# Kernel optimization log

Hardware: AMD Instinct MI355X
Metric: run time of the kernel (lower is better)

## Reference

```python
import jax, jax.numpy as jnp
import numpy as np

N, E, ND, ED, H, OUT, L, VC = 10000, 160000, 8, 4, 128, 256, 6, 6
HEADS, C = 4, 128  # GATConv: out_channels=128 per head, concat=False -> mean over heads


def _ln(x, g, b, eps=1e-5):
    m = x.mean(-1, keepdims=True)
    v = ((x - m) ** 2).mean(-1, keepdims=True)
    return (x - m) * jax.lax.rsqrt(v + eps) * g + b


def _gat_layer(h, src, dst, e_attr, lw, a_src, a_dst, lew, a_edge, bias):
    # h: [N,H]; e_attr: [Etot,H]; PyG GATConv(heads=4, concat=False, edge_dim=H)
    xh = (h @ lw).reshape(N, HEADS, C)                 # [N,4,128]
    eh = (e_attr @ lew).reshape(-1, HEADS, C)          # [Etot,4,128]
    al_s = jnp.einsum('nhc,hc->nh', xh, a_src)
    al_d = jnp.einsum('nhc,hc->nh', xh, a_dst)
    al_e = jnp.einsum('ehc,hc->eh', eh, a_edge)
    alpha = jax.nn.leaky_relu(al_s[src] + al_d[dst] + al_e, 0.2)  # [Etot,4]
    amax = jax.ops.segment_max(alpha, dst, num_segments=N)
    ex = jnp.exp(alpha - amax[dst])
    den = jax.ops.segment_sum(ex, dst, num_segments=N)
    w = ex / (den[dst] + 1e-16)
    out = jax.ops.segment_sum(xh[src] * w[..., None], dst, num_segments=N)  # [N,4,128]
    return out.mean(axis=1) + bias


def setup_inputs() -> dict:
    key = jax.random.key(0)
    ks = jax.random.split(key, 32)
    s = 0.05
    d = {
        'x': jax.random.normal(ks[0], (N, ND), jnp.float32),
        'edge_index': jax.random.randint(ks[1], (2, E), 0, N),
        'edge_attr': jax.random.uniform(ks[2], (E, ED), jnp.float32),
        'vnf_context': jax.random.normal(ks[3], (1, VC), jnp.float32),
        # node embedding
        'node_w': jax.random.normal(ks[4], (ND, H)) * s, 'node_b': jnp.zeros((H,)),
        # EdgeAttentionLayer
        'ea_proj_w': jax.random.normal(ks[5], (ED, H)) * s, 'ea_proj_b': jnp.zeros((H,)),
        'vnf_w': jax.random.normal(ks[6], (VC, H)) * s, 'vnf_b': jnp.zeros((H,)),
        'att1_w': jax.random.normal(ks[7], (2 * H, H)) * s, 'att1_b': jnp.zeros((H,)),
        'att2_w': jax.random.normal(ks[8], (H, H // 2)) * s, 'att2_b': jnp.zeros((H // 2,)),
        'att3_w': jax.random.normal(ks[9], (H // 2, 1)) * s, 'att3_b': jnp.zeros((1,)),
        # per-layer GATConv params (stacked over L layers)
        'gat_lin_w': jax.random.normal(ks[10], (L, H, HEADS * C)) * s,
        'gat_att_src': jax.random.normal(ks[11], (L, HEADS, C)) * s,
        'gat_att_dst': jax.random.normal(ks[12], (L, HEADS, C)) * s,
        'gat_lin_edge_w': jax.random.normal(ks[13], (L, H, HEADS * C)) * s,
        'gat_att_edge': jax.random.normal(ks[14], (L, HEADS, C)) * s,
        'gat_bias': jnp.zeros((L, C)),
        'ln_scale': jnp.ones((L, H)), 'ln_bias': jnp.zeros((L, H)),
        # output projection
        'out_w': jax.random.normal(ks[15], (H, OUT)) * s, 'out_b': jnp.zeros((OUT,)),
    }
    return d


def reference(x, edge_index, edge_attr, vnf_context, node_w, node_b, ea_proj_w, ea_proj_b,
              vnf_w, vnf_b, att1_w, att1_b, att2_w, att2_b, att3_w, att3_b,
              gat_lin_w, gat_att_src, gat_att_dst, gat_lin_edge_w, gat_att_edge, gat_bias,
              ln_scale, ln_bias, out_w, out_b):
    src, dst = edge_index[0], edge_index[1]
    h = x @ node_w + node_b                                   # [N,128]
    # EdgeAttentionLayer (eval mode, no network_state)
    ef = edge_attr @ ea_proj_w + ea_proj_b                    # [E,128]
    vnf = vnf_context @ vnf_w + vnf_b                         # [1,128]
    comb = jnp.concatenate([ef, jnp.broadcast_to(vnf, (E, H))], axis=-1)
    a = jax.nn.relu(comb @ att1_w + att1_b)
    a = jax.nn.relu(a @ att2_w + att2_b)
    e_gate = jax.nn.sigmoid(a @ att3_w + att3_b)              # [E,1]
    w_edge = ef * e_gate                                      # [E,128]
    # GATConv default add_self_loops=True, fill_value='mean'
    loop = jnp.arange(N)
    src2 = jnp.concatenate([src, loop])
    dst2 = jnp.concatenate([dst, loop])
    e2 = jnp.concatenate([w_edge, jnp.broadcast_to(w_edge.mean(0, keepdims=True), (N, H))], axis=0)
    for l in range(L):
        hc = _gat_layer(h, src2, dst2, e2, gat_lin_w[l], gat_att_src[l], gat_att_dst[l],
                        gat_lin_edge_w[l], gat_att_edge[l], gat_bias[l])
        h = _ln(h + jax.nn.relu(hc), ln_scale[l], ln_bias[l])
    return h @ out_w + out_b                                  # [N,256]
```

## Files before the change

### kernel.cpp

```cpp
#include <hip/hip_runtime.h>
#include <hip/hip_bf16.h>
#include <math.h>

#define Nn 10000
#define Ee 160000
#define LL 6

typedef short v8s __attribute__((ext_vector_type(8)));
typedef float v4f __attribute__((ext_vector_type(4)));

__device__ __forceinline__ unsigned short f2bf(float v) {
    unsigned int b = __float_as_uint(v);
    b += 0x7fffu + ((b >> 16) & 1u);
    return (unsigned short)(b >> 16);
}
__device__ __forceinline__ float bflo(unsigned int u) { return __uint_as_float(u << 16); }
__device__ __forceinline__ float bfhi(unsigned int u) { return __uint_as_float(u & 0xffff0000u); }

__global__ __launch_bounds__(256) void k_first(
    const float* __restrict__ x, const float* __restrict__ nw,
    const float* __restrict__ nb, float* __restrict__ h, unsigned short* __restrict__ hb,
    const int* __restrict__ ei, int* __restrict__ hist,
    const float* __restrict__ glw, const float* __restrict__ gas,
    const float* __restrict__ gad, const float* __restrict__ glew,
    const float* __restrict__ gae, float* __restrict__ Bs,
    float* __restrict__ Bd, float* __restrict__ Be,
    unsigned short* __restrict__ WsumT,
    const float* __restrict__ a2w, unsigned short* __restrict__ w2bf,
    const float* __restrict__ ow, unsigned short* __restrict__ owbT,
    const float* __restrict__ vnfc, const float* __restrict__ vw,
    const float* __restrict__ vb, const float* __restrict__ eab,
    const float* __restrict__ a1w, const float* __restrict__ a1b,
    const float* __restrict__ eaw, float* __restrict__ E1) {
    __shared__ float vr[128];
    __shared__ float sM1[512];
    __shared__ float sd1[128];
    int b = blockIdx.x, t = threadIdx.x;
    if (b < 5000) {
        int idx = b * 256 + t;
        int n = idx >> 7, c = idx & 127;
        const float* xr = x + (size_t)n * 8;
        float acc = nb[c];
#pragma unroll
        for (int k = 0; k < 8; k++) acc += xr[k] * nw[k * 128 + c];
        h[idx] = acc;
        hb[idx] = f2bf(acc);
        return;
    }
    if (b < 5625) {
        int i = (b - 5000) * 256 + t;
        atomicAdd(&hist[ei[Ee + i]], 1);
        return;
    }
    if (b < 5637) {
        int idx = (b - 5625) * 256 + t;
        if (idx >= LL * 128 * 4) return;
        int hh = idx & 3, k = (idx >> 2) & 127, l = idx >> 9;
        const float* lwp = glw  + (size_t)l * 65536 + k * 512 + hh * 128;
        const float* lep = glew + (size_t)l * 65536 + k * 512 + hh * 128;
        const float* sp = gas + l * 512 + hh * 128;
        const float* dp = gad + l * 512 + hh * 128;
        const float* ep = gae + l * 512 + hh * 128;
        float s1 = 0, s2 = 0, s3 = 0;
        for (int c = 0; c < 128; c++) {
            float lv = lwp[c];
            s1 += lv * sp[c];
            s2 += lv * dp[c];
            s3 += lep[c] * ep[c];
        }
        Bs[idx] = s1; Bd[idx] = s2; Be[idx] = s3;
        return;
    }
    if (b < 7173) {
        int idx = (b - 5637) * 256 + t;
        int kk = idx & 511;
        int c = (idx >> 9) & 127;
        int l = idx >> 16;
        float v = 0.25f * glw[(size_t)l * 65536 + (size_t)(kk & 127) * 512 + (kk >> 7) * 128 + c];
        WsumT[(size_t)l * 65536 + (size_t)c * 512 + kk] = f2bf(v);
        return;
    }
    if (b < 7205) {
        int idx = (b - 7173) * 256 + t;
        int j = idx & 7, lane = (idx >> 3) & 63, nt = (idx >> 9) & 3, ks = idx >> 11;
        int k = ks * 32 + ((lane >> 4) << 3) + j;
        int n = nt * 16 + (lane & 15);
        w2bf[idx] = f2bf(a2w[k * 64 + n]);
        return;
    }
    if (b < 7333) {
        int idx = (b - 7205) * 256 + t;
        int col = idx >> 7, kk = idx & 127;
        owbT[idx] = f2bf(ow[kk * 256 + col]);
        return;
    }
    {
        if (t < 128) {
            float a = vb[t];
#pragma unroll
            for (int k = 0; k < 6; k++) a += vnfc[k] * vw[k * 128 + t];
            vr[t] = a;
        }
        __syncthreads();
        if (t < 128) {
            float a = a1b[t];
            for (int k = 0; k < 128; k++) a += eab[k] * a1w[k * 128 + t];
            for (int k = 0; k < 128; k++) a += vr[k] * a1w[(128 + k) * 128 + t];
            sd1[t] = a;
        }
#pragma unroll
        for (int rr = 0; rr < 2; rr++) {
            int id = rr * 256 + t;
            int r = id >> 7, j = id & 127;
            float a = 0.f;
            for (int k = 0; k < 128; k++) a += eaw[r * 128 + k] * a1w[k * 128 + j];
            sM1[id] = a;
        }
        __syncthreads();
        if (t < 128) {
            E1[t * 8 + 0] = sM1[t];
            E1[t * 8 + 1] = sM1[128 + t];
            E1[t * 8 + 2] = sM1[256 + t];
            E1[t * 8 + 3] = sM1[384 + t];
            E1[t * 8 + 4] = sd1[t];
            E1[t * 8 + 5] = 0.f; E1[t * 8 + 6] = 0.f; E1[t * 8 + 7] = 0.f;
        }
    }
}

__global__ __launch_bounds__(1024) void k_scan(
    const int* __restrict__ hist, int* __restrict__ seg, int* __restrict__ pos,
    const float* __restrict__ eaw, const float* __restrict__ eab,
    const float* __restrict__ Be, float* __restrict__ PB, float* __restrict__ cB) {
    __shared__ int wsums[16];
    __shared__ int carry_s;
    int t = threadIdx.x;
    if (blockIdx.x == 1) {
        if (t >= 24) return;
        int l = t >> 2, hh = t & 3;
        const float* bp = Be + l * 512 + hh;
        float s0 = 0, s1 = 0, s2 = 0, s3 = 0, sc = 0;
        for (int k = 0; k < 128; k++) {
            float bv = bp[k * 4];
            s0 += eaw[0 * 128 + k] * bv;
            s1 += eaw[1 * 128 + k] * bv;
            s2 += eaw[2 * 128 + k] * bv;
            s3 += eaw[3 * 128 + k] * bv;
            sc += eab[k] * bv;
        }
        PB[0 * 24 + t] = s0; PB[1 * 24 + t] = s1;
        PB[2 * 24 + t] = s2; PB[3 * 24 + t] = s3;
        cB[t] = sc;
        return;
    }
    int lane = t & 63, wid = t >> 6;
    if (t == 0) { carry_s = 0; seg[0] = 0; }
    __syncthreads();
    for (int base = 0; base < Nn; base += 1024) {
        int idx = base + t;
        int v = (idx < Nn) ? hist[idx] : 0;
        int sc = v;
#pragma unroll
        for (int d = 1; d < 64; d <<= 1) {
            int up = __shfl_up(sc, d);
            if (lane >= d) sc += up;
        }
        if (lane == 63) wsums[wid] = sc;
        __syncthreads();
        if (wid == 0) {
            int wv = (lane < 16) ? wsums[lane] : 0;
            int wsc = wv;
#pragma unroll
            for (int d = 1; d < 16; d <<= 1) {
                int up = __shfl_up(wsc, d);
                if (lane >= d) wsc += up;
            }
            if (lane < 16) wsums[lane] = wsc - wv;
        }
        __syncthreads();
        int carry = carry_s;
        int inc = sc + wsums[wid] + carry;
        if (idx < Nn) { seg[idx + 1] = inc; pos[idx] = inc - v; }
        __syncthreads();
        if (t == 1023) carry_s = inc;
        __syncthreads();
    }
}

__global__ __launch_bounds__(256, 2) void k_edge(
    const float* __restrict__ ea, const float* __restrict__ E1,
    const unsigned short* __restrict__ w2bf,
    const float* __restrict__ a2b, const float* __restrict__ a3w,
    const float* __restrict__ a3b,
    const float* __restrict__ PB, const float* __restrict__ cB,
    const int* __restrict__ ei, int* __restrict__ pos, int* __restrict__ srcv,
    float* __restrict__ aleT, float* __restrict__ gsum,
    const float* __restrict__ h, const float* __restrict__ Bs,
    const float* __restrict__ Bd, float* __restrict__ als, float* __restrict__ ald) {
    __shared__ float4 sM[128];
    __shared__ float sD[128];
    __shared__ float4 sevs[256];
    __shared__ float gsh[256];
    __shared__ float sgsum[5];
    int t = threadIdx.x;
    int b = blockIdx.x;
    if (b >= 625) {
        int idx = (b - 625) * 256 + t;
        if (idx >= Nn * 8) return;
        int n = idx >> 3, slot = idx & 7;
        const float* B = (slot < 4) ? Bs : Bd;
        int hh = slot & 3;
        const float4* hr = (const float4*)(h + (size_t)n * 128);
        float s = 0.f;
#pragma unroll 8
        for (int kb = 0; kb < 32; kb++) {
            float4 hv = hr[kb];
            s += hv.x * B[(4 * kb + 0) * 4 + hh] + hv.y * B[(4 * kb + 1) * 4 + hh]
               + hv.z * B[(4 * kb + 2) * 4 + hh] + hv.w * B[(4 * kb + 3) * 4 + hh];
        }
        if (slot < 4) als[n * 4 + hh] = s;
        else          ald[n * 4 + hh] = s;
        return;
    }
    int lane = t & 63;
    int wid = t >> 6;
    int c = lane & 15, q = lane >> 4;
    int eb0 = b * 256;

    int my_src = ei[eb0 + t];
    int my_dst = ei[Ee + eb0 + t];
    sevs[t] = *(const float4*)(ea + (size_t)(eb0 + t) * 4);
    if (t < 128) {
        int slot = t ^ ((t >> 3) & 3);
        sM[slot] = *(const float4*)(E1 + t * 8);
        sD[t] = E1[t * 8 + 4];
    }
    if (t < 5) sgsum[t] = 0.f;
    __syncthreads();

    float4 ev4[4];
#pragma unroll
    for (int mt = 0; mt < 4; mt++) ev4[mt] = sevs[(wid * 4 + mt) * 16 + c];

    v8s av[4][4];
#pragma unroll
    for (int ks = 0; ks < 4; ks++) {
        float4 mr[8]; float dr[8];
#pragma unroll
        for (int j = 0; j < 8; j++) {
            int k = ks * 32 + q * 8 + j;
            mr[j] = sM[k ^ q];
            dr[j] = sD[k];
        }
#pragma unroll
        for (int mt = 0; mt < 4; mt++) {
            float4 ev = ev4[mt];
            v8s a;
#pragma unroll
            for (int j = 0; j < 8; j++) {
                float xv = fmaxf(dr[j] + ev.x * mr[j].x + ev.y * mr[j].y
                                       + ev.z * mr[j].z + ev.w * mr[j].w, 0.f);
                a[j] = (short)f2bf(xv);
            }
            av[mt][ks] = a;
        }
    }

    v4f acc[4][4];
#pragma unroll
    for (int nt = 0; nt < 4; nt++) {
        float bb = a2b[nt * 16 + c];
#pragma unroll
        for (int mt = 0; mt < 4; mt++) acc[mt][nt] = (v4f){bb, bb, bb, bb};
    }
#pragma unroll
    for (int nt = 0; nt < 4; nt++) {
#pragma unroll
        for (int ks = 0; ks < 4; ks++) {
            v8s bfr = *(const v8s*)(w2bf + ((size_t)(ks * 4 + nt) * 64 + lane) * 8);
#pragma unroll
            for (int mt = 0; mt < 4; mt++)
                acc[mt][nt] = __builtin_amdgcn_mfma_f32_16x16x32_bf16(av[mt][ks], bfr, acc[mt][nt], 0, 0, 0);
        }
    }

    float a3r[4];
#pragma unroll
    for (int nt = 0; nt < 4; nt++) a3r[nt] = a3w[nt * 16 + c];
    float a3b0 = a3b[0];
#pragma unroll
    for (int mt = 0; mt < 4; mt++) {
#pragma unroll
        for (int r = 0; r < 4; r++) {
            float s = 0.f;
#pragma unroll
            for (int nt = 0; nt < 4; nt++) s += fmaxf(acc[mt][nt][r], 0.f) * a3r[nt];
            s += __shfl_xor(s, 1); s += __shfl_xor(s, 2);
            s += __shfl_xor(s, 4); s += __shfl_xor(s, 8);
            if (c == 0) gsh[(wid * 4 + mt) * 16 + q * 4 + r] = 1.f / (1.f + __expf(-(s + a3b0)));
        }
    }
    __syncthreads();

    float g = gsh[t];
    float4 evv = sevs[t];
    float v0 = g, v1 = g * evv.x, v2 = g * evv.y, v3 = g * evv.z, v4 = g * evv.w;
#pragma unroll
    for (int d = 32; d > 0; d >>= 1) {
        v0 += __shfl_down(v0, d); v1 += __shfl_down(v1, d); v2 += __shfl_down(v2, d);
        v3 += __shfl_down(v3, d); v4 += __shfl_down(v4, d);
    }
    if (lane == 0) {
        atomicAdd(&sgsum[0], v0); atomicAdd(&sgsum[1], v1); atomicAdd(&sgsum[2], v2);
        atomicAdd(&sgsum[3], v3); atomicAdd(&sgsum[4], v4);
    }
    __syncthreads();
    if (t < 5) atomicAdd(&gsum[t], sgsum[t]);
    int slot = atomicAdd(&pos[my_dst], 1);
    srcv[slot] = my_src;
#pragma unroll
    for (int i4 = 0; i4 < 6; i4++) {
        float4 cc = *(const float4*)(cB + i4 * 4);
        float4 p0 = *(const float4*)(PB + 0 * 24 + i4 * 4);
        float4 p1 = *(const float4*)(PB + 1 * 24 + i4 * 4);
        float4 p2 = *(const float4*)(PB + 2 * 24 + i4 * 4);
        float4 p3 = *(const float4*)(PB + 3 * 24 + i4 * 4);
        float4 o;
        o.x = g * (cc.x + evv.x * p0.x + evv.y * p1.x + evv.z * p2.x + evv.w * p3.x);
        o.y = g * (cc.y + evv.x * p0.y + evv.y * p1.y + evv.z * p2.y + evv.w * p3.y);
        o.z = g * (cc.z + evv.x * p0.z + evv.y * p1.z + evv.z * p2.z + evv.w * p3.z);
        o.w = g * (cc.w + evv.x * p0.w + evv.y * p1.w + evv.z * p2.w + evv.w * p3.w);
        *(float4*)(aleT + (size_t)i4 * Ee * 4 + (size_t)slot * 4) = o;
    }
}

__global__ __launch_bounds__(1024) void k_agg3(
    const int* __restrict__ srcv, const int* __restrict__ seg,
    const float* __restrict__ als, const float* __restrict__ ald,
    const float* __restrict__ aleS_l,
    const unsigned short* __restrict__ hb, unsigned short* __restrict__ aggb,
    const float* __restrict__ gsum, const float* __restrict__ PBl,
    const float* __restrict__ cBl) {
    __shared__ float part[8][512];
    __shared__ float pden[8][4];
    int t = threadIdx.x;
    int lane = t & 63;
    int wv = (t >> 6) & 1;
    int w = t >> 7;
    int n = blockIdx.x * 8 + w;
    int start = seg[n], end = seg[n + 1];
    int deg = end - start;
    int half = (deg + 1) >> 1;
    int s0 = start + wv * half;
    int e0 = wv ? end : start + half;
    int hp = lane >> 4;
    int cch = (lane & 15) * 8;
    float aldh = ald[n * 4 + hp];
    float den = 0.f;
    float4 acc0 = make_float4(0.f, 0.f, 0.f, 0.f);
    float4 acc1 = make_float4(0.f, 0.f, 0.f, 0.f);
    int i = s0;
    for (; i + 4 <= e0; i += 4) {
        int sa = srcv[i], sb = srcv[i + 1], sc = srcv[i + 2], sd = srcv[i + 3];
        float ala = aleS_l[(size_t)(i + 0) * 4 + hp];
        float alb = aleS_l[(size_t)(i + 1) * 4 + hp];
        float alc = aleS_l[(size_t)(i + 2) * 4 + hp];
        float ald_ = aleS_l[(size_t)(i + 3) * 4 + hp];
        float asa = als[sa * 4 + hp], asb = als[sb * 4 + hp];
        float asc = als[sc * 4 + hp], asd = als[sd * 4 + hp];
        uint4 ua = *(const uint4*)(hb + (size_t)sa * 128 + cch);
        uint4 ub = *(const uint4*)(hb + (size_t)sb * 128 + cch);
        uint4 uc = *(const uint4*)(hb + (size_t)sc * 128 + cch);
        uint4 ud = *(const uint4*)(hb + (size_t)sd * 128 + cch);
        float ava = asa + aldh + ala; ava = ava > 0.f ? ava : 0.2f * ava;
        float avb = asb + aldh + alb; avb = avb > 0.f ? avb : 0.2f * avb;
        float avc = asc + aldh + alc; avc = avc > 0.f ? avc : 0.2f * avc;
        float avd = asd + aldh + ald_; avd = avd > 0.f ? avd : 0.2f * avd;
        float ea = __expf(fminf(ava, 60.f));
        float eb = __expf(fminf(avb, 60.f));
        float ec = __expf(fminf(avc, 60.f));
        float ed = __expf(fminf(avd, 60.f));
        den += (ea + eb) + (ec + ed);
        acc0.x += (ea * bflo(ua.x) + eb * bflo(ub.x)) + (ec * bflo(uc.x) + ed * bflo(ud.x));
        acc0.y += (ea * bfhi(ua.x) + eb * bfhi(ub.x)) + (ec * bfhi(uc.x) + ed * bfhi(ud.x));
        acc0.z += (ea * bflo(ua.y) + eb * bflo(ub.y)) + (ec * bflo(uc.y) + ed * bflo(ud.y));
        acc0.w += (ea * bfhi(ua.y) + eb * bfhi(ub.y)) + (ec * bfhi(uc.y) + ed * bfhi(ud.y));
        acc1.x += (ea * bflo(ua.z) + eb * bflo(ub.z)) + (ec * bflo(uc.z) + ed * bflo(ud.z));
        acc1.y += (ea * bfhi(ua.z) + eb * bfhi(ub.z)) + (ec * bfhi(uc.z) + ed * bfhi(ud.z));
        acc1.z += (ea * bflo(ua.w) + eb * bflo(ub.w)) + (ec * bflo(uc.w) + ed * bflo(ud.w));
        acc1.w += (ea * bfhi(ua.w) + eb * bfhi(ub.w)) + (ec * bfhi(uc.w) + ed * bfhi(ud.w));
    }
    for (; i < e0; i++) {
        int sa = srcv[i];
        float ala = aleS_l[(size_t)i * 4 + hp];
        float ava = als[sa * 4 + hp] + aldh + ala;
        ava = ava > 0.f ? ava : 0.2f * ava;
        float ea = __expf(fminf(ava, 60.f));
        den += ea;
        uint4 ua = *(const uint4*)(hb + (size_t)sa * 128 + cch);
        acc0.x += ea * bflo(ua.x); acc0.y += ea * bfhi(ua.x);
        acc0.z += ea * bflo(ua.y); acc0.w += ea * bfhi(ua.y);
        acc1.x += ea * bflo(ua.z); acc1.y += ea * bfhi(ua.z);
        acc1.z += ea * bflo(ua.w); acc1.w += ea * bfhi(ua.w);
    }
    if (wv == 0) {
        float lale = (gsum[0] * cBl[hp] + gsum[1] * PBl[hp] + gsum[2] * PBl[24 + hp]
                    + gsum[3] * PBl[48 + hp] + gsum[4] * PBl[72 + hp]) * (1.0f / Ee);
        float av = als[n * 4 + hp] + aldh + lale;
        av = av > 0.f ? av : 0.2f * av;
        float e0s = __expf(fminf(av, 60.f));
        den += e0s;
        uint4 ua = *(const uint4*)(hb + (size_t)n * 128 + cch);
        acc0.x += e0s * bflo(ua.x); acc0.y += e0s * bfhi(ua.x);
        acc0.z += e0s * bflo(ua.y); acc0.w += e0s * bfhi(ua.y);
        acc1.x += e0s * bflo(ua.z); acc1.y += e0s * bfhi(ua.z);
        acc1.z += e0s * bflo(ua.w); acc1.w += e0s * bfhi(ua.w);
    }
    if (wv == 1) {
        *(float4*)&part[w][lane * 8] = acc0;
        *(float4*)&part[w][lane * 8 + 4] = acc1;
        if ((lane & 15) == 0) pden[w][hp] = den;
    }
    __syncthreads();
    if (wv == 0) {
        float4 p0 = *(const float4*)&part[w][lane * 8];
        float4 p1 = *(const float4*)&part[w][lane * 8 + 4];
        float inv2 = 1.f / (den + pden[w][hp] + 1e-16f);
        acc0.x = (acc0.x + p0.x) * inv2; acc0.y = (acc0.y + p0.y) * inv2;
        acc0.z = (acc0.z + p0.z) * inv2; acc0.w = (acc0.w + p0.w) * inv2;
        acc1.x = (acc1.x + p1.x) * inv2; acc1.y = (acc1.y + p1.y) * inv2;
        acc1.z = (acc1.z + p1.z) * inv2; acc1.w = (acc1.w + p1.w) * inv2;
        ushort4 q0, q1;
        q0.x = f2bf(acc0.x); q0.y = f2bf(acc0.y); q0.z = f2bf(acc0.z); q0.w = f2bf(acc0.w);
        q1.x = f2bf(acc1.x); q1.y = f2bf(acc1.y); q1.z = f2bf(acc1.z); q1.w = f2bf(acc1.w);
        *(ushort4*)(aggb + (size_t)n * 512 + lane * 8) = q0;
        *(ushort4*)(aggb + (size_t)n * 512 + lane * 8 + 4) = q1;
    }
}

__global__ __launch_bounds__(256) void k_post(
    const unsigned short* __restrict__ aggb, const unsigned short* __restrict__ WsumT_l,
    const float* __restrict__ gbias, const float* __restrict__ lnsc,
    const float* __restrict__ lnbi, float* __restrict__ h,
    unsigned short* __restrict__ hb, const float* __restrict__ Bs_n,
    const float* __restrict__ Bd_n, float* __restrict__ als, float* __restrict__ ald,
    const unsigned short* __restrict__ owbT, const float* __restrict__ ob,
    float* __restrict__ out) {
    int t = threadIdx.x;
    int lane = t & 63, w = t >> 6;
    int n0 = (blockIdx.x * 4 + w) * 16;
    if (n0 >= Nn) return;
    int m = lane & 15, q = lane >> 4;
    v4f acc[8];
#pragma unroll
    for (int nt = 0; nt < 8; nt++) acc[nt] = (v4f){0.f, 0.f, 0.f, 0.f};
    const unsigned short* arow = aggb + (size_t)(n0 + m) * 512 + q * 8;
#pragma unroll 4
    for (int ks = 0; ks < 16; ks++) {
        v8s fa = *(const v8s*)(arow + ks * 32);
#pragma unroll
        for (int nt = 0; nt < 8; nt++) {
            int col = nt * 16 + m;
            v8s fb = *(const v8s*)(WsumT_l + (size_t)col * 512 + ks * 32 + q * 8);
            acc[nt] = __builtin_amdgcn_mfma_f32_16x16x32_bf16(fa, fb, acc[nt], 0, 0, 0);
        }
    }
    float v[8][4];
    float s1[4] = {0.f, 0.f, 0.f, 0.f}, s2[4] = {0.f, 0.f, 0.f, 0.f};
#pragma unroll
    for (int nt = 0; nt < 8; nt++) {
        int col = nt * 16 + m;
        float b = gbias[col];
#pragma unroll
        for (int r = 0; r < 4; r++) {
            int row = n0 + q * 4 + r;
            float val = h[(size_t)row * 128 + col] + fmaxf(acc[nt][r] + b, 0.f);
            v[nt][r] = val;
            s1[r] += val; s2[r] += val * val;
        }
    }
#pragma unroll
    for (int d = 1; d <= 8; d <<= 1) {
#pragma unroll
        for (int r = 0; r < 4; r++) {
            s1[r] += __shfl_xor(s1[r], d);
            s2[r] += __shfl_xor(s2[r], d);
        }
    }
    float o8[8][4];
#pragma unroll
    for (int r = 0; r < 4; r++) {
        float mean = s1[r] * (1.f / 128.f);
        float var = s2[r] * (1.f / 128.f) - mean * mean;
        float rinv = rsqrtf(var + 1e-5f);
        int row = n0 + q * 4 + r;
#pragma unroll
        for (int nt = 0; nt < 8; nt++) {
            int col = nt * 16 + m;
            float o = (v[nt][r] - mean) * rinv * lnsc[col] + lnbi[col];
            o8[nt][r] = o;
            h[(size_t)row * 128 + col] = o;
            hb[(size_t)row * 128 + col] = f2bf(o);
        }
    }
    if (owbT == nullptr) {
        float sal[4][4], sad[4][4];
#pragma unroll
        for (int r = 0; r < 4; r++) {
#pragma unroll
            for (int hh = 0; hh < 4; hh++) { sal[r][hh] = 0.f; sad[r][hh] = 0.f; }
        }
#pragma unroll
        for (int nt = 0; nt < 8; nt++) {
            int col = nt * 16 + m;
            float4 bs = *(const float4*)(Bs_n + col * 4);
            float4 bd = *(const float4*)(Bd_n + col * 4);
#pragma unroll
            for (int r = 0; r < 4; r++) {
                float o = o8[nt][r];
                sal[r][0] += o * bs.x; sal[r][1] += o * bs.y;
                sal[r][2] += o * bs.z; sal[r][3] += o * bs.w;
                sad[r][0] += o * bd.x; sad[r][1] += o * bd.y;
                sad[r][2] += o * bd.z; sad[r][3] += o * bd.w;
            }
        }
#pragma unroll
        for (int d = 1; d <= 8; d <<= 1) {
#pragma unroll
            for (int r = 0; r < 4; r++) {
#pragma unroll
                for (int hh = 0; hh < 4; hh++) {
                    sal[r][hh] += __shfl_xor(sal[r][hh], d);
                    sad[r][hh] += __shfl_xor(sad[r][hh], d);
                }
            }
        }
        if (m < 8) {
            int hh = m & 3;
#pragma unroll
            for (int r = 0; r < 4; r++) {
                int row = n0 + q * 4 + r;
                float va = (hh == 0) ? sal[r][0] : (hh == 1) ? sal[r][1] : (hh == 2) ? sal[r][2] : sal[r][3];
                float vd = (hh == 0) ? sad[r][0] : (hh == 1) ? sad[r][1] : (hh == 2) ? sad[r][2] : sad[r][3];
                if (m < 4) als[row * 4 + hh] = va;
                else       ald[row * 4 + hh] = vd;
            }
        }
    } else {
        v4f oacc[16];
#pragma unroll
        for (int ct = 0; ct < 16; ct++) oacc[ct] = (v4f){0.f, 0.f, 0.f, 0.f};
#pragma unroll
        for (int ks = 0; ks < 4; ks++) {
            v8s fa = *(const v8s*)(hb + (size_t)(n0 + m) * 128 + ks * 32 + q * 8);
#pragma unroll
            for (int ct = 0; ct < 16; ct++) {
                v8s fb = *(const v8s*)(owbT + (size_t)(ct * 16 + m) * 128 + ks * 32 + q * 8);
                oacc[ct] = __builtin_amdgcn_mfma_f32_16x16x32_bf16(fa, fb, oacc[ct], 0, 0, 0);
            }
        }
#pragma unroll
        for (int ct = 0; ct < 16; ct++) {
            float obv = ob[ct * 16 + m];
#pragma unroll
            for (int r = 0; r < 4; r++) {
                int row = n0 + q * 4 + r;
                out[(size_t)row * 256 + ct * 16 + m] = oacc[ct][r] + obv;
            }
        }
    }
}

extern "C" void kernel_launch(void* const* d_in, const int* in_sizes, int n_in,
                              void* d_out, int out_size, void* d_ws, size_t ws_size,
                              hipStream_t stream) {
    const float* x    = (const float*)d_in[0];
    const int*   ei   = (const int*)d_in[1];
    const float* ea   = (const float*)d_in[2];
    const float* vnfc = (const float*)d_in[3];
    const float* nw   = (const float*)d_in[4];
    const float* nb   = (const float*)d_in[5];
    const float* eaw  = (const float*)d_in[6];
    const float* eab  = (const float*)d_in[7];
    const float* vw   = (const float*)d_in[8];
    const float* vb   = (const float*)d_in[9];
    const float* a1w  = (const float*)d_in[10];
    const float* a1b  = (const float*)d_in[11];
    const float* a2w  = (const float*)d_in[12];
    const float* a2b  = (const float*)d_in[13];
    const float* a3w  = (const float*)d_in[14];
    const float* a3b  = (const float*)d_in[15];
    const float* glw  = (const float*)d_in[16];
    const float* gas  = (const float*)d_in[17];
    const float* gad  = (const float*)d_in[18];
    const float* glew = (const float*)d_in[19];
    const float* gae  = (const float*)d_in[20];
    const float* gb   = (const float*)d_in[21];
    const float* lnsc = (const float*)d_in[22];
    const float* lnbi = (const float*)d_in[23];
    const float* ow   = (const float*)d_in[24];
    const float* ob   = (const float*)d_in[25];
    float* out = (float*)d_out;

    char* w = (char*)d_ws;
    size_t o = 0;
    auto allocf = [&](size_t cnt) { float* p = (float*)(w + o); o += ((cnt * 4 + 255) / 256) * 256; return p; };
    auto alloci = [&](size_t cnt) { int* p = (int*)(w + o); o += ((cnt * 4 + 255) / 256) * 256; return p; };
    auto allocu = [&](size_t cnt) { unsigned short* p = (unsigned short*)(w + o); o += ((cnt * 2 + 255) / 256) * 256; return p; };
    int* hist     = alloci(Nn);
    float* gsum   = allocf(8);
    float* h      = allocf((size_t)Nn * 128);
    unsigned short* hb    = allocu((size_t)Nn * 128);
    unsigned short* aggb  = allocu((size_t)Nn * 512);
    unsigned short* WsumT = allocu((size_t)LL * 128 * 512);
    unsigned short* w2bf  = allocu(8192);
    unsigned short* owbT  = allocu(32768);
    float* als    = allocf((size_t)Nn * 4);
    float* ald    = allocf((size_t)Nn * 4);
    float* aleT   = allocf((size_t)LL * Ee * 4);
    float* Bs     = allocf(3072);
    float* Bd     = allocf(3072);
    float* Be     = allocf(3072);
    float* E1     = allocf(1024);
    float* PB     = allocf(96);
    float* cB     = allocf(24);
    int* seg      = alloci(Nn + 1);
    int* pos      = alloci(Nn);
    int* srcv     = alloci(Ee);

    hipMemsetAsync(hist, 0, ((size_t)Nn * 4 + 255) / 256 * 256 + 256, stream);

    k_first<<<7334, 256, 0, stream>>>(x, nw, nb, h, hb, ei, hist,
                                      glw, gas, gad, glew, gae, Bs, Bd, Be,
                                      WsumT, a2w, w2bf, ow, owbT, vnfc, vw, vb, eab,
                                      a1w, a1b, eaw, E1);
    k_scan<<<2, 1024, 0, stream>>>(hist, seg, pos, eaw, eab, Be, PB, cB);
    k_edge<<<938, 256, 0, stream>>>(ea, E1, w2bf, a2b, a3w, a3b, PB, cB,
                                    ei, pos, srcv, aleT, gsum, h, Bs, Bd, als, ald);
    for (int l = 0; l < LL; l++) {
        int ln = (l + 1) % LL;
        k_agg3<<<Nn / 8, 1024, 0, stream>>>(srcv, seg, als, ald,
                                            aleT + (size_t)l * Ee * 4, hb, aggb,
                                            gsum, PB + l * 4, cB + l * 4);
        k_post<<<(625 + 3) / 4, 256, 0, stream>>>(aggb, WsumT + (size_t)l * 65536,
                                                  gb + l * 128, lnsc + l * 128, lnbi + l * 128,
                                                  h, hb, Bs + ln * 512, Bd + ln * 512, als, ald,
                                                  (l == LL - 1) ? owbT : (const unsigned short*)nullptr,
                                                  ob, out);
    }
}
```

Baseline: 511.9 us.

## Recompute per-layer edge attention logits in aggregation from stored gate features

Instead of precomputing and storing per-layer edge attention logits for all six layers in the edge kernel, the edge kernel now stores only the gate and gate-weighted edge attributes per sorted edge. Each aggregation launch rebuilds the per-head edge logit with a small dot product against that layer's projection coefficients. This shrinks the edge kernel's write traffic but has each aggregation read a float4 plus a scalar per edge instead of a single float, trading extra reads and FMAs for fewer writes. The aggregation block size also drops from 1024 to 256 threads (2 nodes per block).

Result: faster. 483.6 us (-5.5%).

```diff
diff --git a/kernel.cpp b/kernel.cpp
--- a/kernel.cpp
+++ b/kernel.cpp
@@ -192,9 +192,8 @@
     const unsigned short* __restrict__ w2bf,
     const float* __restrict__ a2b, const float* __restrict__ a3w,
     const float* __restrict__ a3b,
-    const float* __restrict__ PB, const float* __restrict__ cB,
     const int* __restrict__ ei, int* __restrict__ pos, int* __restrict__ srcv,
-    float* __restrict__ aleT, float* __restrict__ gsum,
+    float* __restrict__ gS, float* __restrict__ gevS, float* __restrict__ gsum,
     const float* __restrict__ h, const float* __restrict__ Bs,
     const float* __restrict__ Bd, float* __restrict__ als, float* __restrict__ ald) {
     __shared__ float4 sM[128];
@@ -305,6 +304,7 @@
     float g = gsh[t];
     float4 evv = sevs[t];
     float v0 = g, v1 = g * evv.x, v2 = g * evv.y, v3 = g * evv.z, v4 = g * evv.w;
+    float gw1 = v1, gw2 = v2, gw3 = v3, gw4 = v4;
 #pragma unroll
     for (int d = 32; d > 0; d >>= 1) {
         v0 += __shfl_down(v0, d); v1 += __shfl_down(v1, d); v2 += __shfl_down(v2, d);
@@ -318,36 +318,25 @@
     if (t < 5) atomicAdd(&gsum[t], sgsum[t]);
     int slot = atomicAdd(&pos[my_dst], 1);
     srcv[slot] = my_src;
-#pragma unroll
-    for (int i4 = 0; i4 < 6; i4++) {
-        float4 cc = *(const float4*)(cB + i4 * 4);
-        float4 p0 = *(const float4*)(PB + 0 * 24 + i4 * 4);
-        float4 p1 = *(const float4*)(PB + 1 * 24 + i4 * 4);
-        float4 p2 = *(const float4*)(PB + 2 * 24 + i4 * 4);
-        float4 p3 = *(const float4*)(PB + 3 * 24 + i4 * 4);
-        float4 o;
-        o.x = g * (cc.x + evv.x * p0.x + evv.y * p1.x + evv.z * p2.x + evv.w * p3.x);
-        o.y = g * (cc.y + evv.x * p0.y + evv.y * p1.y + evv.z * p2.y + evv.w * p3.y);
-        o.z = g * (cc.z + evv.x * p0.z + evv.y * p1.z + evv.z * p2.z + evv.w * p3.z);
-        o.w = g * (cc.w + evv.x * p0.w + evv.y * p1.w + evv.z * p2.w + evv.w * p3.w);
-        *(float4*)(aleT + (size_t)i4 * Ee * 4 + (size_t)slot * 4) = o;
-    }
+    gS[slot] = g;
+    float4 gv = make_float4(gw1, gw2, gw3, gw4);
+    *(float4*)(gevS + (size_t)slot * 4) = gv;
 }
 
-__global__ __launch_bounds__(1024) void k_agg3(
+__global__ __launch_bounds__(256) void k_agg3(
     const int* __restrict__ srcv, const int* __restrict__ seg,
     const float* __restrict__ als, const float* __restrict__ ald,
-    const float* __restrict__ aleS_l,
+    const float* __restrict__ gS, const float* __restrict__ gevS,
     const unsigned short* __restrict__ hb, unsigned short* __restrict__ aggb,
     const float* __restrict__ gsum, const float* __restrict__ PBl,
     const float* __restrict__ cBl) {
-    __shared__ float part[8][512];
-    __shared__ float pden[8][4];
+    __shared__ float part[2][512];
+    __shared__ float pden[2][4];
     int t = threadIdx.x;
     int lane = t & 63;
     int wv = (t >> 6) & 1;
     int w = t >> 7;
-    int n = blockIdx.x * 8 + w;
+    int n = blockIdx.x * 2 + w;
     int start = seg[n], end = seg[n + 1];
     int deg = end - start;
     int half = (deg + 1) >> 1;
@@ -355,6 +344,8 @@
     int e0 = wv ? end : start + half;
     int hp = lane >> 4;
     int cch = (lane & 15) * 8;
+    float c0 = cBl[hp];
+    float p0 = PBl[hp], p1 = PBl[24 + hp], p2 = PBl[48 + hp], p3 = PBl[72 + hp];
     float aldh = ald[n * 4 + hp];
     float den = 0.f;
     float4 acc0 = make_float4(0.f, 0.f, 0.f, 0.f);
@@ -362,16 +353,21 @@
     int i = s0;
     for (; i + 4 <= e0; i += 4) {
         int sa = srcv[i], sb = srcv[i + 1], sc = srcv[i + 2], sd = srcv[i + 3];
-        float ala = aleS_l[(size_t)(i + 0) * 4 + hp];
-        float alb = aleS_l[(size_t)(i + 1) * 4 + hp];
-        float alc = aleS_l[(size_t)(i + 2) * 4 + hp];
-        float ald_ = aleS_l[(size_t)(i + 3) * 4 + hp];
+        float ga = gS[i], gb2 = gS[i + 1], gc = gS[i + 2], gd = gS[i + 3];
+        float4 va = *(const float4*)(gevS + (size_t)(i + 0) * 4);
+        float4 vb = *(const float4*)(gevS + (size_t)(i + 1) * 4);
+        float4 vc = *(const float4*)(gevS + (size_t)(i + 2) * 4);
+        float4 vd = *(const float4*)(gevS + (size_t)(i + 3) * 4);
         float asa = als[sa * 4 + hp], asb = als[sb * 4 + hp];
         float asc = als[sc * 4 + hp], asd = als[sd * 4 + hp];
         uint4 ua = *(const uint4*)(hb + (size_t)sa * 128 + cch);
         uint4 ub = *(const uint4*)(hb + (size_t)sb * 128 + cch);
         uint4 uc = *(const uint4*)(hb + (size_t)sc * 128 + cch);
         uint4 ud = *(const uint4*)(hb + (size_t)sd * 128 + cch);
+        float ala = ga * c0 + va.x * p0 + va.y * p1 + va.z * p2 + va.w * p3;
+        float alb = gb2 * c0 + vb.x * p0 + vb.y * p1 + vb.z * p2 + vb.w * p3;
+        float alc = gc * c0 + vc.x * p0 + vc.y * p1 + vc.z * p2 + vc.w * p3;
+        float ald_ = gd * c0 + vd.x * p0 + vd.y * p1 + vd.z * p2 + vd.w * p3;
         float ava = asa + aldh + ala; ava = ava > 0.f ? ava : 0.2f * ava;
         float avb = asb + aldh + alb; avb = avb > 0.f ? avb : 0.2f * avb;
         float avc = asc + aldh + alc; avc = avc > 0.f ? avc : 0.2f * avc;
@@ -392,7 +388,9 @@
     }
     for (; i < e0; i++) {
         int sa = srcv[i];
-        float ala = aleS_l[(size_t)i * 4 + hp];
+        float ga = gS[i];
+        float4 va = *(const float4*)(gevS + (size_t)i * 4);
+        float ala = ga * c0 + va.x * p0 + va.y * p1 + va.z * p2 + va.w * p3;
         float ava = als[sa * 4 + hp] + aldh + ala;
         ava = ava > 0.f ? ava : 0.2f * ava;
         float ea = __expf(fminf(ava, 60.f));
@@ -404,8 +402,8 @@
         acc1.z += ea * bflo(ua.w); acc1.w += ea * bfhi(ua.w);
     }
     if (wv == 0) {
-        float lale = (gsum[0] * cBl[hp] + gsum[1] * PBl[hp] + gsum[2] * PBl[24 + hp]
-                    + gsum[3] * PBl[48 + hp] + gsum[4] * PBl[72 + hp]) * (1.0f / Ee);
+        float lale = (gsum[0] * c0 + gsum[1] * p0 + gsum[2] * p1
+                    + gsum[3] * p2 + gsum[4] * p3) * (1.0f / Ee);
         float av = als[n * 4 + hp] + aldh + lale;
         av = av > 0.f ? av : 0.2f * av;
         float e0s = __expf(fminf(av, 60.f));
@@ -423,13 +421,13 @@
     }
     __syncthreads();
     if (wv == 0) {
-        float4 p0 = *(const float4*)&part[w][lane * 8];
-        float4 p1 = *(const float4*)&part[w][lane * 8 + 4];
+        float4 p0v = *(const float4*)&part[w][lane * 8];
+        float4 p1v = *(const float4*)&part[w][lane * 8 + 4];
         float inv2 = 1.f / (den + pden[w][hp] + 1e-16f);
-        acc0.x = (acc0.x + p0.x) * inv2; acc0.y = (acc0.y + p0.y) * inv2;
-        acc0.z = (acc0.z + p0.z) * inv2; acc0.w = (acc0.w + p0.w) * inv2;
-        acc1.x = (acc1.x + p1.x) * inv2; acc1.y = (acc1.y + p1.y) * inv2;
-        acc1.z = (acc1.z + p1.z) * inv2; acc1.w = (acc1.w + p1.w) * inv2;
+        acc0.x = (acc0.x + p0v.x) * inv2; acc0.y = (acc0.y + p0v.y) * inv2;
+        acc0.z = (acc0.z + p0v.z) * inv2; acc0.w = (acc0.w + p0v.w) * inv2;
+        acc1.x = (acc1.x + p1v.x) * inv2; acc1.y = (acc1.y + p1v.y) * inv2;
+        acc1.z = (acc1.z + p1v.z) * inv2; acc1.w = (acc1.w + p1v.w) * inv2;
         ushort4 q0, q1;
         q0.x = f2bf(acc0.x); q0.y = f2bf(acc0.y); q0.z = f2bf(acc0.z); q0.w = f2bf(acc0.w);
         q1.x = f2bf(acc1.x); q1.y = f2bf(acc1.y); q1.z = f2bf(acc1.z); q1.w = f2bf(acc1.w);
@@ -617,7 +615,8 @@
     unsigned short* owbT  = allocu(32768);
     float* als    = allocf((size_t)Nn * 4);
     float* ald    = allocf((size_t)Nn * 4);
-    float* aleT   = allocf((size_t)LL * Ee * 4);
+    float* gS     = allocf((size_t)Ee);
+    float* gevS   = allocf((size_t)Ee * 4);
     float* Bs     = allocf(3072);
     float* Bd     = allocf(3072);
     float* Be     = allocf(3072);
@@ -635,13 +634,12 @@
                                       WsumT, a2w, w2bf, ow, owbT, vnfc, vw, vb, eab,
                                       a1w, a1b, eaw, E1);
     k_scan<<<2, 1024, 0, stream>>>(hist, seg, pos, eaw, eab, Be, PB, cB);
-    k_edge<<<938, 256, 0, stream>>>(ea, E1, w2bf, a2b, a3w, a3b, PB, cB,
-                                    ei, pos, srcv, aleT, gsum, h, Bs, Bd, als, ald);
+    k_edge<<<938, 256, 0, stream>>>(ea, E1, w2bf, a2b, a3w, a3b,
+                                    ei, pos, srcv, gS, gevS, gsum, h, Bs, Bd, als, ald);
     for (int l = 0; l < LL; l++) {
         int ln = (l + 1) % LL;
-        k_agg3<<<Nn / 8, 1024, 0, stream>>>(srcv, seg, als, ald,
-                                            aleT + (size_t)l * Ee * 4, hb, aggb,
-                                            gsum, PB + l * 4, cB + l * 4);
+        k_agg3<<<Nn / 2, 256, 0, stream>>>(srcv, seg, als, ald, gS, gevS, hb, aggb,
+                                           gsum, PB + l * 4, cB + l * 4);
         k_post<<<(625 + 3) / 4, 256, 0, stream>>>(aggb, WsumT + (size_t)l * 65536,
                                                   gb + l * 128, lnsc + l * 128, lnbi + l * 128,
                                                   h, hb, Bs + ln * 512, Bd + ln * 512, als, ald,
```

## Split edge scatter into separate kernel and process edges in CSR order

Applied to the files above, without the earlier changes.

Moves the destination-bucket scatter and the als/ald projection out of k_edge into a new k_scatter kernel that writes (src, edge id) pairs in sorted slot order. k_edge then processes edges in slot order, gathering edge attributes by id and writing the per-layer edge logits contiguously instead of scattering them. k_agg3 reads sources from the int2 array and now uses 256-thread blocks covering 2 nodes instead of 1024-thread blocks covering 8. This adds a kernel launch and a gather on edge attributes, and the srcv reads become 8-byte strided.

New measurement: 471.5 us. 1.09x faster.

```diff
diff --git a/kernel.cpp b/kernel.cpp
--- a/kernel.cpp
+++ b/kernel.cpp
@@ -187,49 +187,56 @@
     }
 }
 
+__global__ __launch_bounds__(256) void k_scatter(
+    const int* __restrict__ ei, int* __restrict__ pos, int2* __restrict__ pse2,
+    const float* __restrict__ h, const float* __restrict__ Bs,
+    const float* __restrict__ Bd, float* __restrict__ als, float* __restrict__ ald) {
+    int b = blockIdx.x, t = threadIdx.x;
+    if (b < 625) {
+        int i = b * 256 + t;
+        int s = ei[i], d = ei[Ee + i];
+        int slot = atomicAdd(&pos[d], 1);
+        pse2[slot] = make_int2(s, i);
+        return;
+    }
+    int idx = (b - 625) * 256 + t;
+    if (idx >= Nn * 8) return;
+    int n = idx >> 3, slot = idx & 7;
+    const float* B = (slot < 4) ? Bs : Bd;
+    int hh = slot & 3;
+    const float4* hr = (const float4*)(h + (size_t)n * 128);
+    float s = 0.f;
+#pragma unroll 8
+    for (int kb = 0; kb < 32; kb++) {
+        float4 hv = hr[kb];
+        s += hv.x * B[(4 * kb + 0) * 4 + hh] + hv.y * B[(4 * kb + 1) * 4 + hh]
+           + hv.z * B[(4 * kb + 2) * 4 + hh] + hv.w * B[(4 * kb + 3) * 4 + hh];
+    }
+    if (slot < 4) als[n * 4 + hh] = s;
+    else          ald[n * 4 + hh] = s;
+}
+
 __global__ __launch_bounds__(256, 2) void k_edge(
     const float* __restrict__ ea, const float* __restrict__ E1,
     const unsigned short* __restrict__ w2bf,
     const float* __restrict__ a2b, const float* __restrict__ a3w,
     const float* __restrict__ a3b,
     const float* __restrict__ PB, const float* __restrict__ cB,
-    const int* __restrict__ ei, int* __restrict__ pos, int* __restrict__ srcv,
-    float* __restrict__ aleT, float* __restrict__ gsum,
-    const float* __restrict__ h, const float* __restrict__ Bs,
-    const float* __restrict__ Bd, float* __restrict__ als, float* __restrict__ ald) {
+    const int2* __restrict__ pse2,
+    float* __restrict__ aleT, float* __restrict__ gsum) {
     __shared__ float4 sM[128];
     __shared__ float sD[128];
     __shared__ float4 sevs[256];
     __shared__ float gsh[256];
     __shared__ float sgsum[5];
     int t = threadIdx.x;
-    int b = blockIdx.x;
-    if (b >= 625) {
-        int idx = (b - 625) * 256 + t;
-        if (idx >= Nn * 8) return;
-        int n = idx >> 3, slot = idx & 7;
-        const float* B = (slot < 4) ? Bs : Bd;
-        int hh = slot & 3;
-        const float4* hr = (const float4*)(h + (size_t)n * 128);
-        float s = 0.f;
-#pragma unroll 8
-        for (int kb = 0; kb < 32; kb++) {
-            float4 hv = hr[kb];
-            s += hv.x * B[(4 * kb + 0) * 4 + hh] + hv.y * B[(4 * kb + 1) * 4 + hh]
-               + hv.z * B[(4 * kb + 2) * 4 + hh] + hv.w * B[(4 * kb + 3) * 4 + hh];
-        }
-        if (slot < 4) als[n * 4 + hh] = s;
-        else          ald[n * 4 + hh] = s;
-        return;
-    }
     int lane = t & 63;
     int wid = t >> 6;
     int c = lane & 15, q = lane >> 4;
-    int eb0 = b * 256;
-
-    int my_src = ei[eb0 + t];
-    int my_dst = ei[Ee + eb0 + t];
-    sevs[t] = *(const float4*)(ea + (size_t)(eb0 + t) * 4);
+    int sb0 = blockIdx.x * 256;
+
+    int eid = pse2[sb0 + t].y;
+    sevs[t] = *(const float4*)(ea + (size_t)eid * 4);
     if (t < 128) {
         int slot = t ^ ((t >> 3) & 3);
         sM[slot] = *(const float4*)(E1 + t * 8);
@@ -316,8 +323,6 @@
     }
     __syncthreads();
     if (t < 5) atomicAdd(&gsum[t], sgsum[t]);
-    int slot = atomicAdd(&pos[my_dst], 1);
-    srcv[slot] = my_src;
 #pragma unroll
     for (int i4 = 0; i4 < 6; i4++) {
         float4 cc = *(const float4*)(cB + i4 * 4);
@@ -330,24 +335,24 @@
         o.y = g * (cc.y + evv.x * p0.y + evv.y * p1.y + evv.z * p2.y + evv.w * p3.y);
         o.z = g * (cc.z + evv.x * p0.z + evv.y * p1.z + evv.z * p2.z + evv.w * p3.z);
         o.w = g * (cc.w + evv.x * p0.w + evv.y * p1.w + evv.z * p2.w + evv.w * p3.w);
-        *(float4*)(aleT + (size_t)i4 * Ee * 4 + (size_t)slot * 4) = o;
-    }
-}
-
-__global__ __launch_bounds__(1024) void k_agg3(
-    const int* __restrict__ srcv, const int* __restrict__ seg,
+        *(float4*)(aleT + (size_t)i4 * Ee * 4 + (size_t)(sb0 + t) * 4) = o;
+    }
+}
+
+__global__ __launch_bounds__(256) void k_agg3(
+    const int2* __restrict__ pse2, const int* __restrict__ seg,
     const float* __restrict__ als, const float* __restrict__ ald,
     const float* __restrict__ aleS_l,
     const unsigned short* __restrict__ hb, unsigned short* __restrict__ aggb,
     const float* __restrict__ gsum, const float* __restrict__ PBl,
     const float* __restrict__ cBl) {
-    __shared__ float part[8][512];
-    __shared__ float pden[8][4];
+    __shared__ float part[2][512];
+    __shared__ float pden[2][4];
     int t = threadIdx.x;
     int lane = t & 63;
     int wv = (t >> 6) & 1;
     int w = t >> 7;
-    int n = blockIdx.x * 8 + w;
+    int n = blockIdx.x * 2 + w;
     int start = seg[n], end = seg[n + 1];
     int deg = end - start;
     int half = (deg + 1) >> 1;
@@ -361,7 +366,7 @@
     float4 acc1 = make_float4(0.f, 0.f, 0.f, 0.f);
     int i = s0;
     for (; i + 4 <= e0; i += 4) {
-        int sa = srcv[i], sb = srcv[i + 1], sc = srcv[i + 2], sd = srcv[i + 3];
+        int sa = pse2[i].x, sb = pse2[i + 1].x, sc = pse2[i + 2].x, sd = pse2[i + 3].x;
         float ala = aleS_l[(size_t)(i + 0) * 4 + hp];
         float alb = aleS_l[(size_t)(i + 1) * 4 + hp];
         float alc = aleS_l[(size_t)(i + 2) * 4 + hp];
@@ -391,7 +396,7 @@
         acc1.w += (ea * bfhi(ua.w) + eb * bfhi(ub.w)) + (ec * bfhi(uc.w) + ed * bfhi(ud.w));
     }
     for (; i < e0; i++) {
-        int sa = srcv[i];
+        int sa = pse2[i].x;
         float ala = aleS_l[(size_t)i * 4 + hp];
         float ava = als[sa * 4 + hp] + aldh + ala;
         ava = ava > 0.f ? ava : 0.2f * ava;
@@ -626,7 +631,7 @@
     float* cB     = allocf(24);
     int* seg      = alloci(Nn + 1);
     int* pos      = alloci(Nn);
-    int* srcv     = alloci(Ee);
+    int2* pse2    = (int2*)alloci((size_t)Ee * 2);
 
     hipMemsetAsync(hist, 0, ((size_t)Nn * 4 + 255) / 256 * 256 + 256, stream);
 
@@ -635,13 +640,14 @@
                                       WsumT, a2w, w2bf, ow, owbT, vnfc, vw, vb, eab,
                                       a1w, a1b, eaw, E1);
     k_scan<<<2, 1024, 0, stream>>>(hist, seg, pos, eaw, eab, Be, PB, cB);
-    k_edge<<<938, 256, 0, stream>>>(ea, E1, w2bf, a2b, a3w, a3b, PB, cB,
-                                    ei, pos, srcv, aleT, gsum, h, Bs, Bd, als, ald);
+    k_scatter<<<938, 256, 0, stream>>>(ei, pos, pse2, h, Bs, Bd, als, ald);
+    k_edge<<<625, 256, 0, stream>>>(ea, E1, w2bf, a2b, a3w, a3b, PB, cB,
+                                    pse2, aleT, gsum);
     for (int l = 0; l < LL; l++) {
         int ln = (l + 1) % LL;
-        k_agg3<<<Nn / 8, 1024, 0, stream>>>(srcv, seg, als, ald,
-                                            aleT + (size_t)l * Ee * 4, hb, aggb,
-                                            gsum, PB + l * 4, cB + l * 4);
+        k_agg3<<<Nn / 2, 256, 0, stream>>>(pse2, seg, als, ald,
+                                           aleT + (size_t)l * Ee * 4, hb, aggb,
+                                           gsum, PB + l * 4, cB + l * 4);
         k_post<<<(625 + 3) / 4, 256, 0, stream>>>(aggb, WsumT + (size_t)l * 65536,
                                                   gb + l * 128, lnsc + l * 128, lnbi + l * 128,
                                                   h, hb, Bs + ln * 512, Bd + ln * 512, als, ald,
```
